# Performance work log

Measured on AMD Instinct MI355X. Metric: run time of the kernel, lower is better.

Reference implementation:

```python
import jax, jax.numpy as jnp
import numpy as np

K = 3          # spline order
NUM = 32       # grid intervals G
IN_DIM = 256
OUT_DIM = 512
BATCH = 2048


def _b_spline_basis(x, grid, k):
    """Cox-de-Boor recursion. x: (B, I); grid: (I, G+2k+1) -> (B, I, G+k)."""
    xg = x[:, :, None]                      # (B, I, 1)
    g = grid[None, :, :]                    # (1, I, G+2k+1)
    val = ((xg >= g[:, :, :-1]) & (xg < g[:, :, 1:])).astype(x.dtype)
    for p in range(1, k + 1):
        left = (xg - g[:, :, :-(p + 1)]) / (g[:, :, p:-1] - g[:, :, :-(p + 1)])
        right = (g[:, :, p + 1:] - xg) / (g[:, :, p + 1:] - g[:, :, 1:-p])
        val = left * val[:, :, :-1] + right * val[:, :, 1:]
    return val                               # (B, I, G+k)


def setup_inputs() -> dict:
    key = jax.random.key(0)
    k1, k2, k3 = jax.random.split(key, 3)
    x = jax.random.normal(k1, (BATCH, IN_DIM), dtype=jnp.float32)
    # uniform grid on [-1, 1], extended by k knots on each side (extend_grid)
    base = np.linspace(-1.0, 1.0, NUM + 1)
    h = 2.0 / NUM
    ext = np.concatenate([base[0] - h * np.arange(K, 0, -1), base,
                          base[-1] + h * np.arange(1, K + 1)]).astype(np.float32)
    grid = jnp.tile(jnp.asarray(ext)[None, :], (IN_DIM, 1))  # (I, G+2k+1)
    coef = 0.1 * jax.random.normal(k2, (IN_DIM, OUT_DIM, NUM + K), dtype=jnp.float32)
    scale_base = jax.random.normal(k3, (IN_DIM, OUT_DIM), dtype=jnp.float32) / np.sqrt(IN_DIM).astype(np.float32)
    scale_sp = jnp.ones((IN_DIM, OUT_DIM), dtype=jnp.float32) / np.sqrt(IN_DIM).astype(np.float32)
    mask = jnp.ones((IN_DIM, OUT_DIM), dtype=jnp.float32)
    return {"x": x, "grid": grid, "coef": coef,
            "scale_base": scale_base, "scale_sp": scale_sp, "mask": mask}


def reference(x, grid, coef, scale_base, scale_sp, mask):
    base = jax.nn.silu(x)                                   # b(x) residual, (B, I)
    bases = _b_spline_basis(x, grid, K)                     # (B, I, G+k)
    # coef2curve: einsum('ijk,jlk->ijl') in pykan -> (B, I, O)
    y = jnp.einsum('bik,iok->bio', bases, coef)
    y = scale_base[None, :, :] * base[:, :, None] + scale_sp[None, :, :] * y
    y = mask[None, :, :] * y
    return jnp.sum(y, axis=1)                               # (B, O)
```

## Files before the change

### kernel.cpp

```cpp
#include <hip/hip_runtime.h>
#include <math.h>

#define BATCH   2048
#define IN_DIM  256
#define OUT_DIM 512
#define NK      35
#define KS      48
#define BTILE   128
#define OTILE   128
#define ICHUNK  32
#define NSPLIT  8
#define COEFS_BYTES ((size_t)IN_DIM * OUT_DIM * KS * 2)
#define PART_ELEMS  ((size_t)BATCH * OUT_DIM)

__device__ __forceinline__ unsigned short f2bf(float x) {
    unsigned u = __float_as_uint(x);
    u += 0x7FFF + ((u >> 16) & 1);
    return (unsigned short)(u >> 16);
}
__device__ __forceinline__ float bf2f(unsigned short h) {
    return __uint_as_float(((unsigned)h) << 16);
}
__device__ __forceinline__ unsigned pack2(unsigned short a, unsigned short b) {
    return (unsigned)a | ((unsigned)b << 16);
}

typedef __bf16 bf16x8 __attribute__((ext_vector_type(8)));
typedef float  f32x16 __attribute__((ext_vector_type(16)));
typedef unsigned int u32;

__device__ __forceinline__ void gload_lds16(const void* g, void* l) {
    __builtin_amdgcn_global_load_lds((const __attribute__((address_space(1))) u32*)g,
                                     (__attribute__((address_space(3))) u32*)l, 16, 0, 0);
}

#define PR 32
__global__ __launch_bounds__(256) void kan_prep(
    const float* __restrict__ coef,
    const float* __restrict__ scale_base,
    const float* __restrict__ scale_sp,
    const float* __restrict__ mask,
    unsigned short* __restrict__ coefS)
{
    __shared__ float sc[PR * NK];
    __shared__ float sspm[PR], ssbm[PR];
    const int t    = threadIdx.x;
    const int row0 = blockIdx.x * PR;

    {
        const float4* csrc = (const float4*)(coef + (size_t)row0 * NK);
        float4* cdst = (float4*)sc;
        cdst[t] = csrc[t];
        if (t < 24) cdst[t + 256] = csrc[t + 256];
    }
    if (t < PR) {
        float m = mask[row0 + t];
        sspm[t] = scale_sp[row0 + t] * m;
        ssbm[t] = scale_base[row0 + t] * m;
    }
    __syncthreads();

    if (t < PR * 6) {
        int r = t / 6;
        int q = t - r * 6;
        float spm = sspm[r];
        const float* c = sc + r * NK;
        uint4 v = make_uint4(0u, 0u, 0u, 0u);
        if (q < 4) {
            const float* cq = c + q * 8;
            v.x = pack2(f2bf(cq[0] * spm), f2bf(cq[1] * spm));
            v.y = pack2(f2bf(cq[2] * spm), f2bf(cq[3] * spm));
            v.z = pack2(f2bf(cq[4] * spm), f2bf(cq[5] * spm));
            v.w = pack2(f2bf(cq[6] * spm), f2bf(cq[7] * spm));
        } else if (q == 4) {
            float sbm = ssbm[r];
            unsigned short hi = f2bf(sbm);
            unsigned short lo = f2bf(sbm - bf2f(hi));
            v.x = pack2(f2bf(c[32] * spm), f2bf(c[33] * spm));
            v.y = pack2(f2bf(c[34] * spm), 0);
            v.z = pack2(hi, hi);
            v.w = pack2(lo, 0);
        }
        ((uint4*)coefS)[(size_t)(row0 + r) * 6 + q] = v;
    }
}

__global__ __launch_bounds__(256, 2) void kan_mfma(
    const float* __restrict__ x,
    const unsigned short* __restrict__ coefS,
    float* __restrict__ part)
{
    __shared__ __align__(16) short sA[2 * BTILE * KS];
    __shared__ __align__(16) short sB[2 * OTILE * KS];

    const int t    = threadIdx.x;
    const int w    = t >> 6;
    const int lane = t & 63;
    const int l31  = lane & 31, lh = lane >> 5;
    const int wr   = w & 1;
    const int wc   = w >> 1;
    const int o0   = blockIdx.x * OTILE;
    const int b0   = blockIdx.y * BTILE;
    const int ic0  = blockIdx.z * ICHUNK;
    const bool bTh = (t >= 128);
    const int wbase = t & 64;

    {
        uint4 z = make_uint4(0, 0, 0, 0);
        #pragma unroll
        for (int u = 0; u < 6; ++u) {
            int idx = t + 256 * u;
            if (idx < (2 * BTILE * KS * 2) / 16) ((uint4*)sA)[idx] = z;
        }
    }

    f32x16 acc00 = {}, acc01 = {}, acc10 = {}, acc11 = {};

    float xreg = 0.0f;
    int ojb0 = 0, ojb1 = 0;

    auto stageA = [&](short* arow, float xv, int& ojbn) {
        arow[ojbn] = 0; arow[ojbn + 1] = 0; arow[ojbn + 2] = 0; arow[ojbn + 3] = 0;
        float xn = (xv + 1.1875f) * 16.0f;
        float jf = floorf(xn);
        int   j  = (int)jf;
        float u  = xn - jf;
        bool valid = (xn >= 0.0f) && (j <= 37);
        float u2 = u * u, u3 = u2 * u;
        float w0 = (1.0f / 6.0f) * (1.0f - 3.0f * u + 3.0f * u2 - u3);
        float w1 = (1.0f / 6.0f) * (3.0f * u3 - 6.0f * u2 + 4.0f);
        float w2 = (1.0f / 6.0f) * (-3.0f * u3 + 3.0f * u2 + 3.0f * u + 1.0f);
        float w3 = (1.0f / 6.0f) * u3;
        int jb = j - 3;
        if (valid) {
            if ((unsigned)jb       < 35u) arow[jb]     = f2bf(w0);
            if ((unsigned)(jb + 1) < 35u) arow[jb + 1] = f2bf(w1);
            if ((unsigned)(jb + 2) < 35u) arow[jb + 2] = f2bf(w2);
            if ((unsigned)(jb + 3) < 35u) arow[jb + 3] = f2bf(w3);
        }
        ojbn = min(max(jb, 0), 31);
        float sig = 1.0f / (1.0f + __expf(-xv));
        float s   = xv * sig;
        unsigned short shi = f2bf(s);
        unsigned short slo = f2bf(s - bf2f(shi));
        *(unsigned int*)(arow + 36) = pack2(shi, slo);
        arow[38] = shi;
    };

    auto issueB = [&](int i, int buf) {
        const char* gsrc = (const char*)(coefS + ((size_t)i * OUT_DIM + o0) * KS);
        #pragma unroll
        for (int q = 0; q < 6; ++q) {
            int slot = wbase + (t & 63) + 128 * q;
            gload_lds16(gsrc + slot * 16,
                        (void*)(sB + buf * (OTILE * KS) + (wbase + 128 * q) * 8));
        }
    };

    __syncthreads();

    if (!bTh) {
        float x0 = x[(size_t)(b0 + t) * IN_DIM + ic0];
        stageA(sA + t * KS, x0, ojb0);
        xreg = x[(size_t)(b0 + t) * IN_DIM + ic0 + 1];
    } else {
        issueB(ic0, 0);
    }
    __syncthreads();

    auto body = [&](int it, int cur, int nxt, int& ojbn) {
        if (bTh && it + 1 < ICHUNK) issueB(ic0 + it + 1, nxt);

        const short* Ab = sA + cur * (BTILE * KS) + (wr * 64 + l31) * KS + lh * 8;
        const short* Bb = sB + cur * (OTILE * KS) + (wc * 64 + l31) * KS + lh * 8;
        #pragma unroll
        for (int s = 0; s < 3; ++s) {
            bf16x8 a0 = *(const bf16x8*)(Ab + s * 16);
            bf16x8 a1 = *(const bf16x8*)(Ab + 32 * KS + s * 16);
            bf16x8 b0 = *(const bf16x8*)(Bb + s * 16);
            bf16x8 b1 = *(const bf16x8*)(Bb + 32 * KS + s * 16);
            acc00 = __builtin_amdgcn_mfma_f32_32x32x16_bf16(a0, b0, acc00, 0, 0, 0);
            acc01 = __builtin_amdgcn_mfma_f32_32x32x16_bf16(a0, b1, acc01, 0, 0, 0);
            acc10 = __builtin_amdgcn_mfma_f32_32x32x16_bf16(a1, b0, acc10, 0, 0, 0);
            acc11 = __builtin_amdgcn_mfma_f32_32x32x16_bf16(a1, b1, acc11, 0, 0, 0);
        }

        if (!bTh && it + 1 < ICHUNK) {
            stageA(sA + nxt * (BTILE * KS) + t * KS, xreg, ojbn);
            if (it + 2 < ICHUNK)
                xreg = x[(size_t)(b0 + t) * IN_DIM + ic0 + it + 2];
        }
        __syncthreads();
    };

    for (int itp = 0; itp < ICHUNK / 2; ++itp) {
        body(2 * itp,     0, 1, ojb1);
        body(2 * itp + 1, 1, 0, ojb0);
    }

    float* tp = (float*)sA + w * (32 * 36);
    float* pdst = part + (size_t)blockIdx.z * PART_ELEMS;
    #pragma unroll
    for (int r = 0; r < 2; ++r) {
        #pragma unroll
        for (int c = 0; c < 2; ++c) {
            const f32x16& acc = (r == 0) ? ((c == 0) ? acc00 : acc01)
                                         : ((c == 0) ? acc10 : acc11);
            #pragma unroll
            for (int reg = 0; reg < 16; ++reg) {
                int row = (reg & 3) + 8 * (reg >> 2) + 4 * lh;
                tp[row * 36 + l31] = acc[reg];
            }
            int cc = (lane & 7) * 4;
            #pragma unroll
            for (int j = 0; j < 4; ++j) {
                int rr = j * 8 + (lane >> 3);
                float4 v = *(float4*)&tp[rr * 36 + cc];
                int rowg = b0 + wr * 64 + r * 32 + rr;
                int colg = o0 + wc * 64 + c * 32 + cc;
                *(float4*)&pdst[(size_t)rowg * OUT_DIM + colg] = v;
            }
        }
    }
}

__global__ __launch_bounds__(256) void kan_reduce(
    const float4* __restrict__ part, float4* __restrict__ out)
{
    const size_t e = (size_t)blockIdx.x * 256 + threadIdx.x;
    float4 s = part[e];
    #pragma unroll
    for (int z = 1; z < NSPLIT; ++z) {
        float4 v = part[(size_t)z * (PART_ELEMS / 4) + e];
        s.x += v.x; s.y += v.y; s.z += v.z; s.w += v.w;
    }
    out[e] = s;
}

extern "C" void kernel_launch(void* const* d_in, const int* in_sizes, int n_in,
                              void* d_out, int out_size, void* d_ws, size_t ws_size,
                              hipStream_t stream) {
    const float* x          = (const float*)d_in[0];
    const float* coef       = (const float*)d_in[2];
    const float* scale_base = (const float*)d_in[3];
    const float* scale_sp   = (const float*)d_in[4];
    const float* mask       = (const float*)d_in[5];
    unsigned short* coefS   = (unsigned short*)d_ws;
    float* part             = (float*)((char*)d_ws + COEFS_BYTES);

    kan_prep<<<dim3(IN_DIM * OUT_DIM / PR), dim3(256), 0, stream>>>(
        coef, scale_base, scale_sp, mask, coefS);
    kan_mfma<<<dim3(OUT_DIM / OTILE, BATCH / BTILE, NSPLIT), dim3(256), 0, stream>>>(
        x, coefS, part);
    kan_reduce<<<dim3(BATCH * OUT_DIM / 4 / 256), dim3(256), 0, stream>>>(
        (const float4*)part, (float4*)d_out);
}
```

Before: 120.7 us.

## Reorder LDS and packed coefficient layout into k-group-major blocks

Changes the shared-memory layout of the A and B tiles from row-major with a 48-element stride to k-group-major, with 8-element groups across 128 rows. The coefficient pre-pack kernel is changed to write the same blocked layout so the direct global-to-LDS loads fill it. The goal is to remove LDS bank conflicts on the 16-byte MFMA operand reads, since a 96-byte row stride makes lanes collide. A staging thread's scattered 2-byte writes now go to strided addresses, which may cause conflicts on the write side.

```diff
diff --git a/kernel.cpp b/kernel.cpp
--- a/kernel.cpp
+++ b/kernel.cpp
@@ -6,6 +6,7 @@
 #define OUT_DIM 512
 #define NK      35
 #define KS      48
+#define KG      6
 #define BTILE   128
 #define OTILE   128
 #define ICHUNK  32
@@ -81,7 +82,10 @@
             v.z = pack2(hi, hi);
             v.w = pack2(lo, 0);
         }
-        ((uint4*)coefS)[(size_t)(row0 + r) * 6 + q] = v;
+        int g = row0 + r;
+        size_t di = ((size_t)(((g >> 9) * 4 + ((g >> 7) & 3)) * 6 + q)) * 128
+                  + (size_t)(g & 127);
+        ((uint4*)coefS)[di] = v;
     }
 }
 
@@ -119,8 +123,12 @@
     float xreg = 0.0f;
     int ojb0 = 0, ojb1 = 0;
 
-    auto stageA = [&](short* arow, float xv, int& ojbn) {
-        arow[ojbn] = 0; arow[ojbn + 1] = 0; arow[ojbn + 2] = 0; arow[ojbn + 3] = 0;
+    auto stageA = [&](short* abuf, int row, float xv, int& ojbn) {
+        #pragma unroll
+        for (int qq = 0; qq < 4; ++qq) {
+            int k = ojbn + qq;
+            abuf[((k >> 3) * BTILE + row) * 8 + (k & 7)] = 0;
+        }
         float xn = (xv + 1.1875f) * 16.0f;
         float jf = floorf(xn);
         int   j  = (int)jf;
@@ -133,22 +141,32 @@
         float w3 = (1.0f / 6.0f) * u3;
         int jb = j - 3;
         if (valid) {
-            if ((unsigned)jb       < 35u) arow[jb]     = f2bf(w0);
-            if ((unsigned)(jb + 1) < 35u) arow[jb + 1] = f2bf(w1);
-            if ((unsigned)(jb + 2) < 35u) arow[jb + 2] = f2bf(w2);
-            if ((unsigned)(jb + 3) < 35u) arow[jb + 3] = f2bf(w3);
+            if ((unsigned)jb < 35u) {
+                int k = jb;     abuf[((k >> 3) * BTILE + row) * 8 + (k & 7)] = f2bf(w0);
+            }
+            if ((unsigned)(jb + 1) < 35u) {
+                int k = jb + 1; abuf[((k >> 3) * BTILE + row) * 8 + (k & 7)] = f2bf(w1);
+            }
+            if ((unsigned)(jb + 2) < 35u) {
+                int k = jb + 2; abuf[((k >> 3) * BTILE + row) * 8 + (k & 7)] = f2bf(w2);
+            }
+            if ((unsigned)(jb + 3) < 35u) {
+                int k = jb + 3; abuf[((k >> 3) * BTILE + row) * 8 + (k & 7)] = f2bf(w3);
+            }
         }
         ojbn = min(max(jb, 0), 31);
         float sig = 1.0f / (1.0f + __expf(-xv));
         float s   = xv * sig;
         unsigned short shi = f2bf(s);
         unsigned short slo = f2bf(s - bf2f(shi));
-        *(unsigned int*)(arow + 36) = pack2(shi, slo);
-        arow[38] = shi;
+        short* k4 = abuf + (4 * BTILE + row) * 8;
+        *(unsigned int*)(k4 + 4) = pack2(shi, slo);
+        k4[6] = shi;
     };
 
     auto issueB = [&](int i, int buf) {
-        const char* gsrc = (const char*)(coefS + ((size_t)i * OUT_DIM + o0) * KS);
+        const char* gsrc = (const char*)coefS
+                         + ((size_t)i * 4 + (o0 >> 7)) * (KG * OTILE * 8 * 2);
         #pragma unroll
         for (int q = 0; q < 6; ++q) {
             int slot = wbase + (t & 63) + 128 * q;
@@ -161,7 +179,7 @@
 
     if (!bTh) {
         float x0 = x[(size_t)(b0 + t) * IN_DIM + ic0];
-        stageA(sA + t * KS, x0, ojb0);
+        stageA(sA, t, x0, ojb0);
         xreg = x[(size_t)(b0 + t) * IN_DIM + ic0 + 1];
     } else {
         issueB(ic0, 0);
@@ -171,14 +189,14 @@
     auto body = [&](int it, int cur, int nxt, int& ojbn) {
         if (bTh && it + 1 < ICHUNK) issueB(ic0 + it + 1, nxt);
 
-        const short* Ab = sA + cur * (BTILE * KS) + (wr * 64 + l31) * KS + lh * 8;
-        const short* Bb = sB + cur * (OTILE * KS) + (wc * 64 + l31) * KS + lh * 8;
+        const short* Ab = sA + cur * (BTILE * KS) + (lh * BTILE + wr * 64 + l31) * 8;
+        const short* Bb = sB + cur * (OTILE * KS) + (lh * OTILE + wc * 64 + l31) * 8;
         #pragma unroll
         for (int s = 0; s < 3; ++s) {
-            bf16x8 a0 = *(const bf16x8*)(Ab + s * 16);
-            bf16x8 a1 = *(const bf16x8*)(Ab + 32 * KS + s * 16);
-            bf16x8 b0 = *(const bf16x8*)(Bb + s * 16);
-            bf16x8 b1 = *(const bf16x8*)(Bb + 32 * KS + s * 16);
+            bf16x8 a0 = *(const bf16x8*)(Ab + s * (2 * BTILE * 8));
+            bf16x8 a1 = *(const bf16x8*)(Ab + s * (2 * BTILE * 8) + 32 * 8);
+            bf16x8 b0 = *(const bf16x8*)(Bb + s * (2 * OTILE * 8));
+            bf16x8 b1 = *(const bf16x8*)(Bb + s * (2 * OTILE * 8) + 32 * 8);
             acc00 = __builtin_amdgcn_mfma_f32_32x32x16_bf16(a0, b0, acc00, 0, 0, 0);
             acc01 = __builtin_amdgcn_mfma_f32_32x32x16_bf16(a0, b1, acc01, 0, 0, 0);
             acc10 = __builtin_amdgcn_mfma_f32_32x32x16_bf16(a1, b0, acc10, 0, 0, 0);
@@ -186,7 +204,7 @@
         }
 
         if (!bTh && it + 1 < ICHUNK) {
-            stageA(sA + nxt * (BTILE * KS) + t * KS, xreg, ojbn);
+            stageA(sA + nxt * (BTILE * KS), t, xreg, ojbn);
             if (it + 2 < ICHUNK)
                 xreg = x[(size_t)(b0 + t) * IN_DIM + ic0 + it + 2];
         }
```

New measurement: 120.1 us. Within noise of the previous version (-0.5%).

## Precompute compact spline fragments and load MFMA operands directly into registers

Applied to the files above, without the earlier changes.

Moves the per-element spline weight and SiLU computation into the prep kernel, which writes a compact packed record per (input, batch) pair. The MFMA kernel no longer stages A and B tiles in LDS. It loads the coefficient fragments from a re-laid-out global array straight into registers, rebuilds the sparse A fragment in registers with selects, and double-buffers the loads across iterations. This drops the LDS traffic and per-iteration barriers. The costs are extra global reads, since each wave loads its own B fragments and tiles are re-read across waves, higher register pressure, and a linearised grid order that changes L2 locality.

```diff
diff --git a/kernel.cpp b/kernel.cpp
--- a/kernel.cpp
+++ b/kernel.cpp
@@ -12,6 +12,8 @@
 #define NSPLIT  8
 #define COEFS_BYTES ((size_t)IN_DIM * OUT_DIM * KS * 2)
 #define PART_ELEMS  ((size_t)BATCH * OUT_DIM)
+#define XP4_OFF (COEFS_BYTES + (size_t)NSPLIT * PART_ELEMS * 4)
+#define XP2_OFF (XP4_OFF + (size_t)BATCH * IN_DIM * 16)
 
 __device__ __forceinline__ unsigned short f2bf(float x) {
     unsigned u = __float_as_uint(x);
@@ -27,20 +29,26 @@
 
 typedef __bf16 bf16x8 __attribute__((ext_vector_type(8)));
 typedef float  f32x16 __attribute__((ext_vector_type(16)));
-typedef unsigned int u32;
-
-__device__ __forceinline__ void gload_lds16(const void* g, void* l) {
-    __builtin_amdgcn_global_load_lds((const __attribute__((address_space(1))) u32*)g,
-                                     (__attribute__((address_space(3))) u32*)l, 16, 0, 0);
+typedef int    i32x4  __attribute__((ext_vector_type(4)));
+
+__device__ __forceinline__ bf16x8 as_bf16x8(i32x4 v) {
+    bf16x8 r; __builtin_memcpy(&r, &v, 16); return r;
+}
+__device__ __forceinline__ bf16x8 frag_bf(const unsigned u[4]) {
+    i32x4 v; v[0] = u[0]; v[1] = u[1]; v[2] = u[2]; v[3] = u[3];
+    return as_bf16x8(v);
 }
 
 #define PR 32
 __global__ __launch_bounds__(256) void kan_prep(
+    const float* __restrict__ x,
     const float* __restrict__ coef,
     const float* __restrict__ scale_base,
     const float* __restrict__ scale_sp,
     const float* __restrict__ mask,
-    unsigned short* __restrict__ coefS)
+    unsigned short* __restrict__ coefS,
+    uint4* __restrict__ xp4,
+    uint2* __restrict__ xp2)
 {
     __shared__ float sc[PR * NK];
     __shared__ float sspm[PR], ssbm[PR];
@@ -57,6 +65,46 @@
         float m = mask[row0 + t];
         sspm[t] = scale_sp[row0 + t] * m;
         ssbm[t] = scale_base[row0 + t] * m;
+    }
+
+    if (blockIdx.x < (BATCH * IN_DIM) / 256) {
+        int flatT = blockIdx.x * 256 + t;
+        int i = flatT >> 11;
+        int b = flatT & 2047;
+        float xv = x[(size_t)b * IN_DIM + i];
+        float xn = (xv + 1.1875f) * 16.0f;
+        float jf = floorf(xn);
+        int   j  = (int)jf;
+        float u  = xn - jf;
+        bool valid = (xn >= 0.0f) && (j <= 37);
+        float u2 = u * u, u3 = u2 * u;
+        float w0 = (1.0f / 6.0f) * (1.0f - 3.0f * u + 3.0f * u2 - u3);
+        float w1 = (1.0f / 6.0f) * (3.0f * u3 - 6.0f * u2 + 4.0f);
+        float w2 = (1.0f / 6.0f) * (-3.0f * u3 + 3.0f * u2 + 3.0f * u + 1.0f);
+        float w3f = (1.0f / 6.0f) * u3;
+        int jb = j - 3;
+        unsigned short h0 = f2bf(w0), h1 = f2bf(w1), h2 = f2bf(w2), h3 = f2bf(w3f);
+        int  m0  = jb >> 1;
+        bool odd = (jb & 1) != 0;
+        unsigned C0 = odd ? pack2(0, h0)
+                          : (jb == 34 ? pack2(h0, 0) : pack2(h0, h1));
+        unsigned C1 = odd ? (jb == 33 ? pack2(h1, 0) : pack2(h1, h2))
+                          : (jb == 32 ? pack2(h2, 0) : pack2(h2, h3));
+        unsigned C2 = pack2(h3, 0);
+        int e0 = (valid && (m0 >= 0)) ? 1 : 0;
+        int e1 = (valid && (m0 + 1 >= 0) && (jb != 34)) ? 1 : 0;
+        int e2 = (valid && odd && (jb != 33) && (m0 + 2 >= 0)) ? 1 : 0;
+        int sat = min(max(m0, -2), 17);
+        uint4 c;
+        c.x = C0; c.y = C1; c.z = C2;
+        c.w = (unsigned)((sat + 2) | (e0 << 8) | (e1 << 9) | (e2 << 10));
+        float sig = 1.0f / (1.0f + __expf(-xv));
+        float s   = xv * sig;
+        unsigned short shi = f2bf(s);
+        unsigned short slo = f2bf(s - bf2f(shi));
+        uint2 bw; bw.x = pack2(shi, slo); bw.y = pack2(shi, 0);
+        xp4[flatT] = c;
+        xp2[flatT] = bw;
     }
     __syncthreads();
 
@@ -81,17 +129,26 @@
             v.z = pack2(hi, hi);
             v.w = pack2(lo, 0);
         }
-        ((uint4*)coefS)[(size_t)(row0 + r) * 6 + q] = v;
-    }
-}
+        int g = row0 + r;
+        size_t di = ((size_t)(((g >> 9) * 4 + ((g >> 7) & 3)) * 6 + q)) * 128
+                  + (size_t)(g & 127);
+        ((uint4*)coefS)[di] = v;
+    }
+}
+
+struct Pre {
+    uint4 c0, c1;
+    uint2 e0, e1;
+    i32x4 B[3][2];
+};
 
 __global__ __launch_bounds__(256, 2) void kan_mfma(
-    const float* __restrict__ x,
+    const uint4* __restrict__ xp4,
+    const uint2* __restrict__ xp2,
     const unsigned short* __restrict__ coefS,
     float* __restrict__ part)
 {
-    __shared__ __align__(16) short sA[2 * BTILE * KS];
-    __shared__ __align__(16) short sB[2 * OTILE * KS];
+    __shared__ __align__(16) float tp_s[4 * 32 * 36];
 
     const int t    = threadIdx.x;
     const int w    = t >> 6;
@@ -99,107 +156,85 @@
     const int l31  = lane & 31, lh = lane >> 5;
     const int wr   = w & 1;
     const int wc   = w >> 1;
-    const int o0   = blockIdx.x * OTILE;
-    const int b0   = blockIdx.y * BTILE;
-    const int ic0  = blockIdx.z * ICHUNK;
-    const bool bTh = (t >= 128);
-    const int wbase = t & 64;
-
-    {
-        uint4 z = make_uint4(0, 0, 0, 0);
-        #pragma unroll
-        for (int u = 0; u < 6; ++u) {
-            int idx = t + 256 * u;
-            if (idx < (2 * BTILE * KS * 2) / 16) ((uint4*)sA)[idx] = z;
-        }
-    }
+
+    const int f   = blockIdx.x;
+    const int z   = f & 7;
+    const int y   = (f >> 3) & 15;
+    const int ot  = f >> 7;
+    const int o0  = ot * OTILE;
+    const int b0  = y * BTILE;
+    const int ic0 = z * ICHUNK;
+
+    const int rA0 = wr * 64 + l31;
+
+    auto loadPre = [&](int i, Pre& P) {
+        size_t xi = (size_t)(ic0 + i) * 2048 + (size_t)(b0 + rA0);
+        P.c0 = xp4[xi];       P.e0 = xp2[xi];
+        P.c1 = xp4[xi + 32];  P.e1 = xp2[xi + 32];
+        const char* bb = (const char*)coefS
+                       + (size_t)((ic0 + i) * 4 + ot) * 12288
+                       + (size_t)lh * 2048 + (size_t)(wc * 64 + l31) * 16;
+        #pragma unroll
+        for (int s = 0; s < 3; ++s) {
+            P.B[s][0] = *(const i32x4*)(bb + s * 4096);
+            P.B[s][1] = *(const i32x4*)(bb + s * 4096 + 512);
+        }
+    };
+
+    auto build3 = [&](uint4 c, uint2 bwv, unsigned fr[3][4]) {
+        int m0 = (int)(c.w & 255u) - 2;
+        int t0 = (c.w & 256u)  ? m0     : 0x40000000;
+        int t1 = (c.w & 512u)  ? m0 + 1 : 0x40000000;
+        int t2 = (c.w & 1024u) ? m0 + 2 : 0x40000000;
+        #pragma unroll
+        for (int s = 0; s < 3; ++s) {
+            int pb = 8 * s + 4 * lh;
+            #pragma unroll
+            for (int q = 0; q < 4; ++q) {
+                int p = pb + q;
+                unsigned v = 0;
+                if (s == 2 && q == 2) v = (lh == 0) ? bwv.x : 0u;
+                if (s == 2 && q == 3) v = (lh == 0) ? bwv.y : 0u;
+                v = (p == t0) ? c.x : v;
+                v = (p == t1) ? c.y : v;
+                v = (p == t2) ? c.z : v;
+                fr[s][q] = v;
+            }
+        }
+    };
 
     f32x16 acc00 = {}, acc01 = {}, acc10 = {}, acc11 = {};
 
-    float xreg = 0.0f;
-    int ojb0 = 0, ojb1 = 0;
-
-    auto stageA = [&](short* arow, float xv, int& ojbn) {
-        arow[ojbn] = 0; arow[ojbn + 1] = 0; arow[ojbn + 2] = 0; arow[ojbn + 3] = 0;
-        float xn = (xv + 1.1875f) * 16.0f;
-        float jf = floorf(xn);
-        int   j  = (int)jf;
-        float u  = xn - jf;
-        bool valid = (xn >= 0.0f) && (j <= 37);
-        float u2 = u * u, u3 = u2 * u;
-        float w0 = (1.0f / 6.0f) * (1.0f - 3.0f * u + 3.0f * u2 - u3);
-        float w1 = (1.0f / 6.0f) * (3.0f * u3 - 6.0f * u2 + 4.0f);
-        float w2 = (1.0f / 6.0f) * (-3.0f * u3 + 3.0f * u2 + 3.0f * u + 1.0f);
-        float w3 = (1.0f / 6.0f) * u3;
-        int jb = j - 3;
-        if (valid) {
-            if ((unsigned)jb       < 35u) arow[jb]     = f2bf(w0);
-            if ((unsigned)(jb + 1) < 35u) arow[jb + 1] = f2bf(w1);
-            if ((unsigned)(jb + 2) < 35u) arow[jb + 2] = f2bf(w2);
-            if ((unsigned)(jb + 3) < 35u) arow[jb + 3] = f2bf(w3);
-        }
-        ojbn = min(max(jb, 0), 31);
-        float sig = 1.0f / (1.0f + __expf(-xv));
-        float s   = xv * sig;
-        unsigned short shi = f2bf(s);
-        unsigned short slo = f2bf(s - bf2f(shi));
-        *(unsigned int*)(arow + 36) = pack2(shi, slo);
-        arow[38] = shi;
+    Pre p0, p1;
+    loadPre(0, p0);
+
+    auto body = [&](int i, Pre& cur, Pre& nxt) {
+        if (i + 1 < ICHUNK) loadPre(i + 1, nxt);
+
+        unsigned fa[3][4], fb[3][4];
+        build3(cur.c0, cur.e0, fa);
+        build3(cur.c1, cur.e1, fb);
+
+        #pragma unroll
+        for (int s = 0; s < 3; ++s) {
+            bf16x8 a0 = frag_bf(fa[s]);
+            bf16x8 a1 = frag_bf(fb[s]);
+            bf16x8 b0v = as_bf16x8(cur.B[s][0]);
+            bf16x8 b1v = as_bf16x8(cur.B[s][1]);
+            acc00 = __builtin_amdgcn_mfma_f32_32x32x16_bf16(a0, b0v, acc00, 0, 0, 0);
+            acc01 = __builtin_amdgcn_mfma_f32_32x32x16_bf16(a0, b1v, acc01, 0, 0, 0);
+            acc10 = __builtin_amdgcn_mfma_f32_32x32x16_bf16(a1, b0v, acc10, 0, 0, 0);
+            acc11 = __builtin_amdgcn_mfma_f32_32x32x16_bf16(a1, b1v, acc11, 0, 0, 0);
+        }
     };
 
-    auto issueB = [&](int i, int buf) {
-        const char* gsrc = (const char*)(coefS + ((size_t)i * OUT_DIM + o0) * KS);
-        #pragma unroll
-        for (int q = 0; q < 6; ++q) {
-            int slot = wbase + (t & 63) + 128 * q;
-            gload_lds16(gsrc + slot * 16,
-                        (void*)(sB + buf * (OTILE * KS) + (wbase + 128 * q) * 8));
-        }
-    };
-
-    __syncthreads();
-
-    if (!bTh) {
-        float x0 = x[(size_t)(b0 + t) * IN_DIM + ic0];
-        stageA(sA + t * KS, x0, ojb0);
-        xreg = x[(size_t)(b0 + t) * IN_DIM + ic0 + 1];
-    } else {
-        issueB(ic0, 0);
-    }
-    __syncthreads();
-
-    auto body = [&](int it, int cur, int nxt, int& ojbn) {
-        if (bTh && it + 1 < ICHUNK) issueB(ic0 + it + 1, nxt);
-
-        const short* Ab = sA + cur * (BTILE * KS) + (wr * 64 + l31) * KS + lh * 8;
-        const short* Bb = sB + cur * (OTILE * KS) + (wc * 64 + l31) * KS + lh * 8;
-        #pragma unroll
-        for (int s = 0; s < 3; ++s) {
-            bf16x8 a0 = *(const bf16x8*)(Ab + s * 16);
-            bf16x8 a1 = *(const bf16x8*)(Ab + 32 * KS + s * 16);
-            bf16x8 b0 = *(const bf16x8*)(Bb + s * 16);
-            bf16x8 b1 = *(const bf16x8*)(Bb + 32 * KS + s * 16);
-            acc00 = __builtin_amdgcn_mfma_f32_32x32x16_bf16(a0, b0, acc00, 0, 0, 0);
-            acc01 = __builtin_amdgcn_mfma_f32_32x32x16_bf16(a0, b1, acc01, 0, 0, 0);
-            acc10 = __builtin_amdgcn_mfma_f32_32x32x16_bf16(a1, b0, acc10, 0, 0, 0);
-            acc11 = __builtin_amdgcn_mfma_f32_32x32x16_bf16(a1, b1, acc11, 0, 0, 0);
-        }
-
-        if (!bTh && it + 1 < ICHUNK) {
-            stageA(sA + nxt * (BTILE * KS) + t * KS, xreg, ojbn);
-            if (it + 2 < ICHUNK)
-                xreg = x[(size_t)(b0 + t) * IN_DIM + ic0 + it + 2];
-        }
-        __syncthreads();
-    };
-
     for (int itp = 0; itp < ICHUNK / 2; ++itp) {
-        body(2 * itp,     0, 1, ojb1);
-        body(2 * itp + 1, 1, 0, ojb0);
-    }
-
-    float* tp = (float*)sA + w * (32 * 36);
-    float* pdst = part + (size_t)blockIdx.z * PART_ELEMS;
+        body(2 * itp,     p0, p1);
+        body(2 * itp + 1, p1, p0);
+    }
+
+    float* tp = tp_s + w * (32 * 36);
+    float* pdst = part + (size_t)z * PART_ELEMS;
     #pragma unroll
     for (int r = 0; r < 2; ++r) {
         #pragma unroll
@@ -247,11 +282,13 @@
     const float* mask       = (const float*)d_in[5];
     unsigned short* coefS   = (unsigned short*)d_ws;
     float* part             = (float*)((char*)d_ws + COEFS_BYTES);
+    uint4* xp4              = (uint4*)((char*)d_ws + XP4_OFF);
+    uint2* xp2              = (uint2*)((char*)d_ws + XP2_OFF);
 
     kan_prep<<<dim3(IN_DIM * OUT_DIM / PR), dim3(256), 0, stream>>>(
-        coef, scale_base, scale_sp, mask, coefS);
-    kan_mfma<<<dim3(OUT_DIM / OTILE, BATCH / BTILE, NSPLIT), dim3(256), 0, stream>>>(
-        x, coefS, part);
+        x, coef, scale_base, scale_sp, mask, coefS, xp4, xp2);
+    kan_mfma<<<dim3(OUT_DIM / OTILE * BATCH / BTILE * NSPLIT), dim3(256), 0, stream>>>(
+        xp4, xp2, coefS, part);
     kan_reduce<<<dim3(BATCH * OUT_DIM / 4 / 256), dim3(256), 0, stream>>>(
         (const float4*)part, (float4*)d_out);
 }
```

Result: slower. 125.4 us (+3.9%).
